# Kernel optimization log

Hardware: AMD Instinct MI355X
Metric: run time of the kernel (lower is better)

Reference implementation:

```python
import jax, jax.numpy as jnp
import numpy as np

D_MODEL = 2048
N_HEAD = 16
HEAD_DIM = D_MODEL // N_HEAD
FFN_DIM = 4 * D_MODEL
B, T = 2, 2048
EPS = float(np.finfo(np.float32).eps)  # torch nn.RMSNorm default eps


def _rmsnorm(x, w):
    return x * jax.lax.rsqrt(jnp.mean(x * x, axis=-1, keepdims=True) + EPS) * w


def _apply_rope(x, cos, sin):
    # x: (B,H,T,hd); cos/sin: (T,hd) with each frequency repeated twice
    cos_pair = cos[..., 0::2]
    sin_pair = sin[..., 0::2]
    x_even = x[..., 0::2]
    x_odd = x[..., 1::2]
    rot_even = x_even * cos_pair - x_odd * sin_pair
    rot_odd = x_odd * cos_pair + x_even * sin_pair
    # interleave back: (..., hd//2, 2) -> (..., hd)
    return jnp.stack([rot_even, rot_odd], axis=-1).reshape(x.shape)


def setup_inputs() -> dict:
    key = jax.random.key(0)
    ks = jax.random.split(key, 9)
    x = jax.random.normal(ks[0], (B, T, D_MODEL), dtype=jnp.float32)
    # real RoPE cache: freqs repeated twice along last axis (interleaved-pair)
    inv_freq = 1.0 / (10000.0 ** (np.arange(0, HEAD_DIM, 2, dtype=np.float32) / HEAD_DIM))
    ang = np.arange(T, dtype=np.float32)[:, None] * inv_freq[None, :]  # (T, hd/2)
    ang2 = np.repeat(ang, 2, axis=-1)  # (T, hd)
    rope_cache = jnp.stack([jnp.cos(jnp.asarray(ang2)), jnp.sin(jnp.asarray(ang2))], axis=0)
    s = 0.02
    return {
        "x": x,
        "rope_cache": rope_cache,
        "attn_norm_w": jnp.ones((D_MODEL,), jnp.float32),
        "qkv_w": s * jax.random.normal(ks[1], (3 * D_MODEL, D_MODEL), jnp.float32),
        "q_norm_w": jnp.ones((HEAD_DIM,), jnp.float32),
        "k_norm_w": jnp.ones((HEAD_DIM,), jnp.float32),
        "out_proj_w": s * jax.random.normal(ks[2], (D_MODEL, D_MODEL), jnp.float32),
        "mlp_norm_w": jnp.ones((D_MODEL,), jnp.float32),
        "mlp_in_w": s * jax.random.normal(ks[3], (FFN_DIM, D_MODEL), jnp.float32),
        "mlp_out_w": s * jax.random.normal(ks[4], (D_MODEL, FFN_DIM), jnp.float32),
    }


def reference(x, rope_cache, attn_norm_w, qkv_w, q_norm_w, k_norm_w,
              out_proj_w, mlp_norm_w, mlp_in_w, mlp_out_w):
    cos, sin = rope_cache[0], rope_cache[1]
    b, t, d = x.shape
    h = _rmsnorm(x, attn_norm_w)
    qkv = h @ qkv_w.T  # (B,T,3D)
    q, k, v = jnp.split(qkv, 3, axis=-1)
    q = q.reshape(b, t, N_HEAD, HEAD_DIM).transpose(0, 2, 1, 3)
    k = k.reshape(b, t, N_HEAD, HEAD_DIM).transpose(0, 2, 1, 3)
    v = v.reshape(b, t, N_HEAD, HEAD_DIM).transpose(0, 2, 1, 3)
    q = _rmsnorm(_apply_rope(q, cos, sin), q_norm_w)
    k = _rmsnorm(_apply_rope(k, cos, sin), k_norm_w)
    scale = 1.0 / jnp.sqrt(jnp.float32(HEAD_DIM))
    scores = jnp.einsum('bhqd,bhkd->bhqk', q, k) * scale
    causal = jnp.tril(jnp.ones((t, t), dtype=bool))
    scores = jnp.where(causal, scores, -jnp.inf)
    attn = jax.nn.softmax(scores, axis=-1)
    attn_out = jnp.einsum('bhqk,bhkd->bhqd', attn, v)
    attn_out = attn_out.transpose(0, 2, 1, 3).reshape(b, t, d)
    x = x + attn_out @ out_proj_w.T
    m = _rmsnorm(x, mlp_norm_w) @ mlp_in_w.T
    m = jnp.square(jax.nn.relu(m))
    return x + m @ mlp_out_w.T
```

## Files before the change

### kernel.cpp

```cpp
#include <hip/hip_runtime.h>
#include <stdint.h>

#define TT 2048
#define DM 2048
#define NH 16
#define HD 128
#define FFN 8192
#define MR 4096
#define EPSF 1.1920928955078125e-07f
#define NEGBIG (-1.0e30f)

typedef __attribute__((ext_vector_type(8))) short short8;
typedef __attribute__((ext_vector_type(4))) float f32x4;
typedef unsigned short u16;
typedef unsigned int u32;

__device__ __forceinline__ float bf2f(u32 u) {
    return __uint_as_float((u & 0xffffu) << 16);
}
__device__ __forceinline__ u16 f2bf(float f) {
    u32 x = __float_as_uint(f);
    return (u16)((x + 0x7fffu + ((x >> 16) & 1u)) >> 16);
}
__device__ __forceinline__ void load8f(const u16* p, float* v) {
    uint4 d = *(const uint4*)p;
    v[0] = bf2f(d.x); v[1] = bf2f(d.x >> 16);
    v[2] = bf2f(d.y); v[3] = bf2f(d.y >> 16);
    v[4] = bf2f(d.z); v[5] = bf2f(d.z >> 16);
    v[6] = bf2f(d.w); v[7] = bf2f(d.w >> 16);
}
__device__ __forceinline__ void load8f32(const float* p, float* v) {
    float4 a = *(const float4*)p, b = *(const float4*)(p + 4);
    v[0]=a.x; v[1]=a.y; v[2]=a.z; v[3]=a.w; v[4]=b.x; v[5]=b.y; v[6]=b.z; v[7]=b.w;
}
__device__ __forceinline__ void store8bf(u16* p, const float* v) {
    uint4 o;
    o.x = (u32)f2bf(v[0]) | ((u32)f2bf(v[1]) << 16);
    o.y = (u32)f2bf(v[2]) | ((u32)f2bf(v[3]) << 16);
    o.z = (u32)f2bf(v[4]) | ((u32)f2bf(v[5]) << 16);
    o.w = (u32)f2bf(v[6]) | ((u32)f2bf(v[7]) << 16);
    *(uint4*)p = o;
}
__device__ __forceinline__ uint4 cvt8_f32_bf16(const float* p) {
    float4 a = *(const float4*)p, b = *(const float4*)(p + 4);
    uint4 o;
    o.x = (u32)f2bf(a.x) | ((u32)f2bf(a.y) << 16);
    o.y = (u32)f2bf(a.z) | ((u32)f2bf(a.w) << 16);
    o.z = (u32)f2bf(b.x) | ((u32)f2bf(b.y) << 16);
    o.w = (u32)f2bf(b.z) | ((u32)f2bf(b.w) << 16);
    return o;
}
__device__ __forceinline__ void gload_lds16(const void* g, void* l) {
    __builtin_amdgcn_global_load_lds((const __attribute__((address_space(1))) u32*)g,
                                     (__attribute__((address_space(3))) u32*)l, 16, 0, 0);
}

__global__ __launch_bounds__(256)
void cvt_w(const float* __restrict__ S, u16* __restrict__ D) {
    size_t i = ((size_t)blockIdx.x * 256 + threadIdx.x) * 8;
    *(uint4*)(D + i) = cvt8_f32_bf16(S + i);
}

__global__ __launch_bounds__(256)
void rmsnorm_k(const float* __restrict__ X, const float* __restrict__ W, u16* __restrict__ O) {
    const int row = blockIdx.x, tid = threadIdx.x;
    float v[8];
    load8f32(X + (size_t)row * DM + tid * 8, v);
    float ssq = 0.f;
#pragma unroll
    for (int i = 0; i < 8; ++i) ssq += v[i] * v[i];
#pragma unroll
    for (int d = 1; d < 64; d <<= 1) ssq += __shfl_xor(ssq, d);
    __shared__ float red[4];
    if ((tid & 63) == 0) red[tid >> 6] = ssq;
    __syncthreads();
    ssq = red[0] + red[1] + red[2] + red[3];
    const float inv = rsqrtf(ssq * (1.f / DM) + EPSF);
    float wv[8], o[8];
    load8f32(W + tid * 8, wv);
#pragma unroll
    for (int i = 0; i < 8; ++i) o[i] = v[i] * inv * wv[i];
    store8bf(O + (size_t)row * DM + tid * 8, o);
}

template<int EPI>
__global__ __launch_bounds__(256)
void gemm_bt(const u16* __restrict__ A, const u16* __restrict__ Bw,
             const float* __restrict__ Res, void* __restrict__ Cp,
             int M, int N, int K, int ldb) {
    __shared__ alignas(16) u16 As[128 * 32];
    __shared__ alignas(16) u16 Bs[128 * 32];
    const int tid = threadIdx.x;
    const int lane = tid & 63, w = tid >> 6;
    const int quad = lane >> 4, col = lane & 15;
    const int n0 = blockIdx.x * 128, m0 = blockIdx.y * 128;
    const int wm = (w >> 1) * 64, wn = (w & 1) * 64;

    const int c0 = tid, c1 = tid + 256;
    const int ar0 = c0 >> 2, aq0 = (c0 & 3) ^ ((ar0 >> 1) & 3);
    const int ar1 = c1 >> 2, aq1 = (c1 & 3) ^ ((ar1 >> 1) & 3);
    const u16* agp0 = A  + (size_t)(m0 + ar0) * K + aq0 * 8;
    const u16* agp1 = A  + (size_t)(m0 + ar1) * K + aq1 * 8;
    const u16* bgp0 = Bw + (size_t)(n0 + ar0) * ldb + aq0 * 8;
    const u16* bgp1 = Bw + (size_t)(n0 + ar1) * ldb + aq1 * 8;
    u16* al0 = As + c0 * 8; u16* al1 = As + c1 * 8;
    u16* bl0 = Bs + c0 * 8; u16* bl1 = Bs + c1 * 8;

    int aoff[4], boff[4];
#pragma unroll
    for (int i = 0; i < 4; ++i) {
        int r = wm + i * 16 + col;
        aoff[i] = r * 32 + (quad ^ ((r >> 1) & 3)) * 8;
        r = wn + i * 16 + col;
        boff[i] = r * 32 + (quad ^ ((r >> 1) & 3)) * 8;
    }

    f32x4 acc[4][4];
#pragma unroll
    for (int i = 0; i < 4; ++i)
#pragma unroll
        for (int j = 0; j < 4; ++j) acc[i][j] = (f32x4){0.f, 0.f, 0.f, 0.f};

    for (int kt = 0; kt < K; kt += 32) {
        __syncthreads();
        gload_lds16(agp0 + kt, al0);
        gload_lds16(agp1 + kt, al1);
        gload_lds16(bgp0 + kt, bl0);
        gload_lds16(bgp1 + kt, bl1);
        __syncthreads();
        short8 af[4], bfr[4];
#pragma unroll
        for (int i = 0; i < 4; ++i) af[i] = *(const short8*)(As + aoff[i]);
#pragma unroll
        for (int i = 0; i < 4; ++i) bfr[i] = *(const short8*)(Bs + boff[i]);
#pragma unroll
        for (int mi = 0; mi < 4; ++mi)
#pragma unroll
            for (int ni = 0; ni < 4; ++ni)
                acc[mi][ni] = __builtin_amdgcn_mfma_f32_16x16x32_bf16(af[mi], bfr[ni], acc[mi][ni], 0, 0, 0);
    }

#pragma unroll
    for (int mi = 0; mi < 4; ++mi)
#pragma unroll
        for (int ni = 0; ni < 4; ++ni) {
            const int rbase = m0 + wm + mi * 16 + quad * 4;
            const int cc = n0 + wn + ni * 16 + col;
#pragma unroll
            for (int rr = 0; rr < 4; ++rr) {
                float v = acc[mi][ni][rr];
                size_t idx = (size_t)(rbase + rr) * N + cc;
                if (EPI == 0) ((u16*)Cp)[idx] = f2bf(v);
                else if (EPI == 1) { float t = fmaxf(v, 0.f); ((u16*)Cp)[idx] = f2bf(t * t); }
                else ((float*)Cp)[idx] = v + Res[idx];
            }
        }
}

template<int EPI>
__global__ __launch_bounds__(512, 2)
void gemm_big(const u16* __restrict__ A, const u16* __restrict__ Bw,
              void* __restrict__ Cp, int M, int N, int K, int ldb) {
    __shared__ alignas(16) u16 As[4][256 * 32];
    __shared__ alignas(16) u16 Bs[4][256 * 32];
    const int tid = threadIdx.x;
    const int lane = tid & 63, w = tid >> 6;
    const int wr = w >> 2, wc = w & 3;
    const int quad = lane >> 4, colL = lane & 15;

    const int nbx = N >> 8;
    const int nwg = gridDim.x;
    const int cpx = nwg >> 3;
    const int bid = blockIdx.x;
    const int swz = (bid & 7) * cpx + (bid >> 3);
    const int by = swz / nbx, bx = swz - by * nbx;
    const int m0 = by << 8, n0 = bx << 8;

    const int r0 = tid >> 2,       q0 = (tid & 3) ^ ((r0 >> 1) & 3);
    const int p1 = tid + 512;
    const int r1 = p1 >> 2,        q1 = (p1 & 3) ^ ((r1 >> 1) & 3);
    const u16* agp0 = A  + (size_t)(m0 + r0) * K   + q0 * 8;
    const u16* agp1 = A  + (size_t)(m0 + r1) * K   + q1 * 8;
    const u16* bgp0 = Bw + (size_t)(n0 + r0) * ldb + q0 * 8;
    const u16* bgp1 = Bw + (size_t)(n0 + r1) * ldb + q1 * 8;
    const int l0 = tid * 8, l1 = p1 * 8;

    int aoff[8], boff[4];
#pragma unroll
    for (int mi = 0; mi < 8; ++mi) {
        int r = wr * 128 + mi * 16 + colL;
        aoff[mi] = r * 32 + (quad ^ ((r >> 1) & 3)) * 8;
    }
#pragma unroll
    for (int ni = 0; ni < 4; ++ni) {
        int r = wc * 64 + ni * 16 + colL;
        boff[ni] = r * 32 + (quad ^ ((r >> 1) & 3)) * 8;
    }

    f32x4 acc[8][4];
#pragma unroll
    for (int i = 0; i < 8; ++i)
#pragma unroll
        for (int j = 0; j < 4; ++j) acc[i][j] = (f32x4){0.f, 0.f, 0.f, 0.f};

    const int KT = K >> 5;

#define GB_STAGE(s) { const int _b = (s) & 3; const size_t _ko = (size_t)(s) * 32; \
    gload_lds16(agp0 + _ko, &As[_b][l0]); \
    gload_lds16(agp1 + _ko, &As[_b][l1]); \
    gload_lds16(bgp0 + _ko, &Bs[_b][l0]); \
    gload_lds16(bgp1 + _ko, &Bs[_b][l1]); }

    GB_STAGE(0);
    GB_STAGE(1);
    GB_STAGE(2);

    for (int t = 0; t < KT; ++t) {
        const int rem = KT - 1 - t;
        if (rem >= 2)      asm volatile("s_waitcnt vmcnt(8)" ::: "memory");
        else if (rem == 1) asm volatile("s_waitcnt vmcnt(4)" ::: "memory");
        else               asm volatile("s_waitcnt vmcnt(0)" ::: "memory");
        __builtin_amdgcn_s_barrier();
        if (t + 3 < KT) GB_STAGE(t + 3);
        const u16* ab = As[t & 3];
        const u16* bb = Bs[t & 3];
        short8 af[8], bfr[4];
#pragma unroll
        for (int mi = 0; mi < 8; ++mi) af[mi] = *(const short8*)(ab + aoff[mi]);
#pragma unroll
        for (int ni = 0; ni < 4; ++ni) bfr[ni] = *(const short8*)(bb + boff[ni]);
        __builtin_amdgcn_s_setprio(1);
#pragma unroll
        for (int mi = 0; mi < 8; ++mi)
#pragma unroll
            for (int ni = 0; ni < 4; ++ni)
                acc[mi][ni] = __builtin_amdgcn_mfma_f32_16x16x32_bf16(af[mi], bfr[ni], acc[mi][ni], 0, 0, 0);
        __builtin_amdgcn_s_setprio(0);
        __builtin_amdgcn_sched_barrier(0);
    }
#undef GB_STAGE

#pragma unroll
    for (int mi = 0; mi < 8; ++mi)
#pragma unroll
        for (int ni = 0; ni < 4; ++ni) {
            const int rbase = m0 + wr * 128 + mi * 16 + quad * 4;
            const int cc = n0 + wc * 64 + ni * 16 + colL;
#pragma unroll
            for (int rr = 0; rr < 4; ++rr) {
                float v = acc[mi][ni][rr];
                size_t idx = (size_t)(rbase + rr) * N + cc;
                if (EPI == 0) ((u16*)Cp)[idx] = f2bf(v);
                else { float tq = fmaxf(v, 0.f); ((u16*)Cp)[idx] = f2bf(tq * tq); }
            }
        }
}

__global__ __launch_bounds__(256)
void rope_split_k(const u16* __restrict__ QKV, const float* __restrict__ RC,
                  const float* __restrict__ QW, const float* __restrict__ KW,
                  u16* __restrict__ Qo, u16* __restrict__ Ko, u16* __restrict__ Vo) {
    const int row = blockIdx.x;
    const int t = row & (TT - 1), b = row >> 11;
    const int tid = threadIdx.x, h = tid >> 4, j = tid & 15;
    const size_t qb = (size_t)row * (3 * DM) + h * HD + j * 8;
    float q[8], k[8], cs[8], sn[8];
    load8f(QKV + qb, q);
    load8f(QKV + qb + DM, k);
    uint4 vv = *(const uint4*)(QKV + qb + 2 * DM);
    load8f32(RC + (size_t)t * HD + j * 8, cs);
    load8f32(RC + (size_t)(TT + t) * HD + j * 8, sn);
    float qr[8], kr[8];
#pragma unroll
    for (int p = 0; p < 4; ++p) {
        float c = cs[2 * p], s = sn[2 * p];
        qr[2*p]   = q[2*p]   * c - q[2*p+1] * s;
        qr[2*p+1] = q[2*p+1] * c + q[2*p]   * s;
        kr[2*p]   = k[2*p]   * c - k[2*p+1] * s;
        kr[2*p+1] = k[2*p+1] * c + k[2*p]   * s;
    }
    float sq = 0.f, sk = 0.f;
#pragma unroll
    for (int i = 0; i < 8; ++i) { sq += qr[i] * qr[i]; sk += kr[i] * kr[i]; }
#pragma unroll
    for (int d = 1; d < 16; d <<= 1) { sq += __shfl_xor(sq, d); sk += __shfl_xor(sk, d); }
    const float iq = rsqrtf(sq * (1.f / HD) + EPSF);
    const float ik = rsqrtf(sk * (1.f / HD) + EPSF);
    float qw[8], kw[8], oq[8], ok[8];
    load8f32(QW + j * 8, qw); load8f32(KW + j * 8, kw);
#pragma unroll
    for (int i = 0; i < 8; ++i) { oq[i] = qr[i] * iq * qw[i]; ok[i] = kr[i] * ik * kw[i]; }
    const size_t ob = ((size_t)(b * NH + h) * TT + t) * HD + j * 8;
    store8bf(Qo + ob, oq);
    store8bf(Ko + ob, ok);
    *(uint4*)(Vo + ob) = vv;
}

__global__ __launch_bounds__(256)
void transpose_v(const u16* __restrict__ V, u16* __restrict__ Vt) {
    __shared__ alignas(16) u16 tile[64][72];
    const int bh = blockIdx.z;
    const int t0 = blockIdx.x * 64, d0 = blockIdx.y * 64;
    const int tid = threadIdx.x;
#pragma unroll
    for (int i = 0; i < 2; ++i) {
        int c = i * 256 + tid;
        int r = c >> 3, cc = (c & 7) * 8;
        *(uint4*)(&tile[r][cc]) = *(const uint4*)(V + ((size_t)bh * TT + t0 + r) * HD + d0 + cc);
    }
    __syncthreads();
#pragma unroll
    for (int i = 0; i < 2; ++i) {
        int c = i * 256 + tid;
        int dc = c >> 3, rr = (c & 7) * 8;
        u16 tmp[8];
#pragma unroll
        for (int kk = 0; kk < 8; ++kk) tmp[kk] = tile[rr + kk][dc];
        uint4 o;
        o.x = (u32)tmp[0] | ((u32)tmp[1] << 16);
        o.y = (u32)tmp[2] | ((u32)tmp[3] << 16);
        o.z = (u32)tmp[4] | ((u32)tmp[5] << 16);
        o.w = (u32)tmp[6] | ((u32)tmp[7] << 16);
        *(uint4*)(Vt + ((size_t)bh * HD + d0 + dc) * TT + t0 + rr) = o;
    }
}

__global__ __launch_bounds__(256)
void attn_k(const u16* __restrict__ Q, const u16* __restrict__ Kg,
            const u16* __restrict__ Vt, u16* __restrict__ O) {
    __shared__ alignas(16) u16 k_lds[2][64 * 128];
    __shared__ alignas(16) u16 v_lds[2][128 * 64];
    __shared__ alignas(16) u16 p_lds[4 * 16 * 72];
    const int qt = gridDim.x - 1 - blockIdx.x;
    const int bh = blockIdx.y;
    const int tid = threadIdx.x, lane = tid & 63, w = tid >> 6;
    const int quad = lane >> 4, col = lane & 15;
    const int qbase = qt * 64;
    const int qrow = qbase + w * 16 + col;

    short8 qf[4];
    const u16* qp = Q + ((size_t)bh * TT + qrow) * HD;
#pragma unroll
    for (int s = 0; s < 4; ++s) qf[s] = *(const short8*)(qp + s * 32 + quad * 8);

    const u16* kp[4]; const u16* vp[4];
#pragma unroll
    for (int i = 0; i < 4; ++i) {
        int lin = i * 256 + tid;
        int r = lin >> 4, sl = lin & 15;
        int gq = sl ^ (r & 15);
        kp[i] = Kg + ((size_t)bh * TT + r) * HD + gq * 8;
    }
#pragma unroll
    for (int i = 0; i < 4; ++i) {
        int lin = i * 256 + tid;
        int r = lin >> 3, sl = lin & 7;
        int gq = sl ^ (r & 7);
        vp[i] = Vt + ((size_t)bh * HD + r) * TT + gq * 8;
    }

    f32x4 oacc[8];
#pragma unroll
    for (int i = 0; i < 8; ++i) oacc[i] = (f32x4){0.f, 0.f, 0.f, 0.f};
    float mrow[4] = {NEGBIG, NEGBIG, NEGBIG, NEGBIG};
    float lrow[4] = {0.f, 0.f, 0.f, 0.f};
    const float scale = 0.08838834764831845f;

    u16* kcur = k_lds[0]; u16* knxt = k_lds[1];
    u16* vcur = v_lds[0]; u16* vnxt = v_lds[1];
#pragma unroll
    for (int i = 0; i < 4; ++i) gload_lds16(kp[i], kcur + (i * 256 + tid) * 8);
#pragma unroll
    for (int i = 0; i < 4; ++i) gload_lds16(vp[i], vcur + (i * 256 + tid) * 8);

    for (int kt = 0; kt <= qt; ++kt) {
        const int kb = kt * 64;
        __syncthreads();

        if (kt < qt) {
            const int kb2 = kb + 64;
#pragma unroll
            for (int i = 0; i < 4; ++i) gload_lds16(kp[i] + (size_t)kb2 * HD, knxt + (i * 256 + tid) * 8);
#pragma unroll
            for (int i = 0; i < 4; ++i) gload_lds16(vp[i] + kb2, vnxt + (i * 256 + tid) * 8);
        }

        f32x4 sfr[4];
#pragma unroll
        for (int ni = 0; ni < 4; ++ni) sfr[ni] = (f32x4){0.f, 0.f, 0.f, 0.f};
        __builtin_amdgcn_s_setprio(1);
#pragma unroll
        for (int ni = 0; ni < 4; ++ni) {
            const int r = ni * 16 + col;
#pragma unroll
            for (int s = 0; s < 4; ++s) {
                int sl = (s * 4 + quad) ^ (r & 15);
                short8 kf = *(const short8*)(kcur + r * 128 + sl * 8);
                sfr[ni] = __builtin_amdgcn_mfma_f32_16x16x32_bf16(qf[s], kf, sfr[ni], 0, 0, 0);
            }
        }
        __builtin_amdgcn_s_setprio(0);
        const bool diag = (kt == qt);
#pragma unroll
        for (int ni = 0; ni < 4; ++ni) {
            const int key = kb + ni * 16 + col;
#pragma unroll
            for (int rr = 0; rr < 4; ++rr) {
                float v = sfr[ni][rr] * scale;
                int qv = qbase + w * 16 + quad * 4 + rr;
                if (diag && key > qv) v = NEGBIG;
                sfr[ni][rr] = v;
            }
        }
        float mx[4];
#pragma unroll
        for (int rr = 0; rr < 4; ++rr)
            mx[rr] = fmaxf(fmaxf(sfr[0][rr], sfr[1][rr]), fmaxf(sfr[2][rr], sfr[3][rr]));
#pragma unroll
        for (int d = 1; d < 16; d <<= 1)
#pragma unroll
            for (int rr = 0; rr < 4; ++rr) mx[rr] = fmaxf(mx[rr], __shfl_xor(mx[rr], d));
        if (__any((mx[0] > mrow[0]) || (mx[1] > mrow[1]) ||
                  (mx[2] > mrow[2]) || (mx[3] > mrow[3]))) {
#pragma unroll
            for (int rr = 0; rr < 4; ++rr) {
                float mn = fmaxf(mrow[rr], mx[rr]);
                float a = __expf(mrow[rr] - mn);
                mrow[rr] = mn;
                lrow[rr] *= a;
#pragma unroll
                for (int i = 0; i < 8; ++i) oacc[i][rr] *= a;
            }
        }
        float rs[4] = {0.f, 0.f, 0.f, 0.f};
#pragma unroll
        for (int ni = 0; ni < 4; ++ni)
#pragma unroll
            for (int rr = 0; rr < 4; ++rr) {
                float p = __expf(sfr[ni][rr] - mrow[rr]);
                sfr[ni][rr] = p;
                rs[rr] += p;
            }
#pragma unroll
        for (int d = 1; d < 16; d <<= 1)
#pragma unroll
            for (int rr = 0; rr < 4; ++rr) rs[rr] += __shfl_xor(rs[rr], d);
#pragma unroll
        for (int rr = 0; rr < 4; ++rr) lrow[rr] += rs[rr];
#pragma unroll
        for (int ni = 0; ni < 4; ++ni)
#pragma unroll
            for (int rr = 0; rr < 4; ++rr)
                p_lds[(w * 16 + quad * 4 + rr) * 72 + ni * 16 + col] = f2bf(sfr[ni][rr]);
        __builtin_amdgcn_s_setprio(1);
#pragma unroll
        for (int ks = 0; ks < 2; ++ks) {
            short8 pa = *(const short8*)(p_lds + (w * 16 + col) * 72 + ks * 32 + quad * 8);
#pragma unroll
            for (int di = 0; di < 8; ++di) {
                int r = di * 16 + col;
                int sl = (ks * 4 + quad) ^ (r & 7);
                short8 vb = *(const short8*)(vcur + r * 64 + sl * 8);
                oacc[di] = __builtin_amdgcn_mfma_f32_16x16x32_bf16(pa, vb, oacc[di], 0, 0, 0);
            }
        }
        __builtin_amdgcn_s_setprio(0);
        { u16* t = kcur; kcur = knxt; knxt = t; }
        { u16* t = vcur; vcur = vnxt; vnxt = t; }
    }
    const int b = bh >> 4, h = bh & 15;
#pragma unroll
    for (int di = 0; di < 8; ++di)
#pragma unroll
        for (int rr = 0; rr < 4; ++rr) {
            int trow = qbase + w * 16 + quad * 4 + rr;
            float ov = oacc[di][rr] / lrow[rr];
            O[((size_t)(b * TT + trow)) * DM + h * HD + di * 16 + col] = f2bf(ov);
        }
}

extern "C" void kernel_launch(void* const* d_in, const int* in_sizes, int n_in,
                              void* d_out, int out_size, void* d_ws, size_t ws_size,
                              hipStream_t stream) {
    const float* x    = (const float*)d_in[0];
    const float* rc   = (const float*)d_in[1];
    const float* anw  = (const float*)d_in[2];
    const float* qkvw = (const float*)d_in[3];
    const float* qnw  = (const float*)d_in[4];
    const float* knw  = (const float*)d_in[5];
    const float* opw  = (const float*)d_in[6];
    const float* mnw  = (const float*)d_in[7];
    const float* miw  = (const float*)d_in[8];
    const float* mow  = (const float*)d_in[9];

    char* ws = (char*)d_ws;
    u16* hbuf = (u16*)(ws);
    u16* Wq   = (u16*)(ws + (16ll  << 20));
    u16* Wmi  = (u16*)(ws + (16ll  << 20));
    u16* vt   = (u16*)(ws + (16ll  << 20));
    u16* aout = (u16*)(ws + (32ll  << 20));
    u16* Wmo  = (u16*)(ws + (48ll  << 20));
    u16* qkv  = (u16*)(ws + (48ll  << 20));
    u16* mbuf = (u16*)(ws + (80ll  << 20));
    u16* qh   = (u16*)(ws + (96ll  << 20));
    u16* Wo   = (u16*)(ws + (112ll << 20));
    u16* kh   = (u16*)(ws + (112ll << 20));
    u16* vh   = (u16*)(ws);
    float* xo = (float*)d_out;

    rmsnorm_k<<<MR, 256, 0, stream>>>(x, anw, hbuf);
    cvt_w<<<6144, 256, 0, stream>>>(qkvw, Wq);
    gemm_big<0><<<384, 512, 0, stream>>>(hbuf, Wq, qkv, MR, 3 * DM, DM, DM);
    rope_split_k<<<MR, 256, 0, stream>>>(qkv, rc, qnw, knw, qh, kh, vh);
    transpose_v<<<dim3(32, 2, 32), 256, 0, stream>>>(vh, vt);
    attn_k<<<dim3(32, 32), 256, 0, stream>>>(qh, kh, vt, aout);
    cvt_w<<<2048, 256, 0, stream>>>(opw, Wo);
    cvt_w<<<8192, 256, 0, stream>>>(mow, Wmo);
    gemm_bt<2><<<dim3(16, 32), 256, 0, stream>>>(aout, Wo, x, xo, MR, DM, DM, DM);
    rmsnorm_k<<<MR, 256, 0, stream>>>(xo, mnw, hbuf);
    cvt_w<<<8192, 256, 0, stream>>>(miw, Wmi);
    gemm_big<1><<<256, 512, 0, stream>>>(hbuf, Wmi, mbuf, MR, FFN / 2, DM, DM);
    gemm_bt<2><<<dim3(16, 32), 256, 0, stream>>>(mbuf, Wmo, xo, xo, MR, DM, FFN / 2, FFN);
    gemm_big<1><<<256, 512, 0, stream>>>(hbuf, Wmi + (size_t)(FFN / 2) * DM, mbuf, MR, FFN / 2, DM, DM);
    gemm_bt<2><<<dim3(16, 32), 256, 0, stream>>>(mbuf, Wmo + FFN / 2, xo, xo, MR, DM, FFN / 2, FFN);
}
```

Baseline: 1.047 ms.

## Pipeline residual GEMMs with 4-stage LDS ring and enlarge attention query tile

```diff
diff --git a/kernel.cpp b/kernel.cpp
--- a/kernel.cpp
+++ b/kernel.cpp
@@ -84,12 +84,12 @@
 }
 
 template<int EPI>
-__global__ __launch_bounds__(256)
-void gemm_bt(const u16* __restrict__ A, const u16* __restrict__ Bw,
-             const float* __restrict__ Res, void* __restrict__ Cp,
-             int M, int N, int K, int ldb) {
-    __shared__ alignas(16) u16 As[128 * 32];
-    __shared__ alignas(16) u16 Bs[128 * 32];
+__global__ __launch_bounds__(256, 2)
+void gemm_ring(const u16* __restrict__ A, const u16* __restrict__ Bw,
+               const float* __restrict__ Res, void* __restrict__ Cp,
+               int M, int N, int K, int ldb) {
+    __shared__ alignas(16) u16 As[4][128 * 32];
+    __shared__ alignas(16) u16 Bs[4][128 * 32];
     const int tid = threadIdx.x;
     const int lane = tid & 63, w = tid >> 6;
     const int quad = lane >> 4, col = lane & 15;
@@ -103,8 +103,7 @@
     const u16* agp1 = A  + (size_t)(m0 + ar1) * K + aq1 * 8;
     const u16* bgp0 = Bw + (size_t)(n0 + ar0) * ldb + aq0 * 8;
     const u16* bgp1 = Bw + (size_t)(n0 + ar1) * ldb + aq1 * 8;
-    u16* al0 = As + c0 * 8; u16* al1 = As + c1 * 8;
-    u16* bl0 = Bs + c0 * 8; u16* bl1 = Bs + c1 * 8;
+    const int l0 = c0 * 8, l1 = c1 * 8;
 
     int aoff[4], boff[4];
 #pragma unroll
@@ -121,24 +120,42 @@
 #pragma unroll
         for (int j = 0; j < 4; ++j) acc[i][j] = (f32x4){0.f, 0.f, 0.f, 0.f};
 
-    for (int kt = 0; kt < K; kt += 32) {
-        __syncthreads();
-        gload_lds16(agp0 + kt, al0);
-        gload_lds16(agp1 + kt, al1);
-        gload_lds16(bgp0 + kt, bl0);
-        gload_lds16(bgp1 + kt, bl1);
-        __syncthreads();
+    const int KT = K >> 5;
+
+#define GR_STAGE(s) { const int _b = (s) & 3; const size_t _ko = (size_t)(s) * 32; \
+    gload_lds16(agp0 + _ko, &As[_b][l0]); \
+    gload_lds16(agp1 + _ko, &As[_b][l1]); \
+    gload_lds16(bgp0 + _ko, &Bs[_b][l0]); \
+    gload_lds16(bgp1 + _ko, &Bs[_b][l1]); }
+
+    GR_STAGE(0);
+    GR_STAGE(1);
+    GR_STAGE(2);
+
+    for (int t = 0; t < KT; ++t) {
+        const int rem = KT - 1 - t;
+        if (rem >= 2)      asm volatile("s_waitcnt vmcnt(8)" ::: "memory");
+        else if (rem == 1) asm volatile("s_waitcnt vmcnt(4)" ::: "memory");
+        else               asm volatile("s_waitcnt vmcnt(0)" ::: "memory");
+        __builtin_amdgcn_s_barrier();
+        if (t + 3 < KT) GR_STAGE(t + 3);
+        const u16* ab = As[t & 3];
+        const u16* bb = Bs[t & 3];
         short8 af[4], bfr[4];
 #pragma unroll
-        for (int i = 0; i < 4; ++i) af[i] = *(const short8*)(As + aoff[i]);
-#pragma unroll
-        for (int i = 0; i < 4; ++i) bfr[i] = *(const short8*)(Bs + boff[i]);
+        for (int i = 0; i < 4; ++i) af[i] = *(const short8*)(ab + aoff[i]);
+#pragma unroll
+        for (int i = 0; i < 4; ++i) bfr[i] = *(const short8*)(bb + boff[i]);
+        __builtin_amdgcn_s_setprio(1);
 #pragma unroll
         for (int mi = 0; mi < 4; ++mi)
 #pragma unroll
             for (int ni = 0; ni < 4; ++ni)
                 acc[mi][ni] = __builtin_amdgcn_mfma_f32_16x16x32_bf16(af[mi], bfr[ni], acc[mi][ni], 0, 0, 0);
-    }
+        __builtin_amdgcn_s_setprio(0);
+        __builtin_amdgcn_sched_barrier(0);
+    }
+#undef GR_STAGE
 
 #pragma unroll
     for (int mi = 0; mi < 4; ++mi)
@@ -151,7 +168,7 @@
                 float v = acc[mi][ni][rr];
                 size_t idx = (size_t)(rbase + rr) * N + cc;
                 if (EPI == 0) ((u16*)Cp)[idx] = f2bf(v);
-                else if (EPI == 1) { float t = fmaxf(v, 0.f); ((u16*)Cp)[idx] = f2bf(t * t); }
+                else if (EPI == 1) { float t2 = fmaxf(v, 0.f); ((u16*)Cp)[idx] = f2bf(t2 * t2); }
                 else ((float*)Cp)[idx] = v + Res[idx];
             }
         }
@@ -325,23 +342,26 @@
     }
 }
 
-__global__ __launch_bounds__(256)
+__global__ __launch_bounds__(256, 2)
 void attn_k(const u16* __restrict__ Q, const u16* __restrict__ Kg,
             const u16* __restrict__ Vt, u16* __restrict__ O) {
     __shared__ alignas(16) u16 k_lds[2][64 * 128];
     __shared__ alignas(16) u16 v_lds[2][128 * 64];
-    __shared__ alignas(16) u16 p_lds[4 * 16 * 72];
+    __shared__ alignas(16) u16 p_lds[128 * 40];
     const int qt = gridDim.x - 1 - blockIdx.x;
     const int bh = blockIdx.y;
     const int tid = threadIdx.x, lane = tid & 63, w = tid >> 6;
     const int quad = lane >> 4, col = lane & 15;
-    const int qbase = qt * 64;
-    const int qrow = qbase + w * 16 + col;
-
-    short8 qf[4];
-    const u16* qp = Q + ((size_t)bh * TT + qrow) * HD;
-#pragma unroll
-    for (int s = 0; s < 4; ++s) qf[s] = *(const short8*)(qp + s * 32 + quad * 8);
+    const int qbase = qt * 128;
+    const int wq = qbase + w * 32;
+
+    short8 qf[2][4];
+#pragma unroll
+    for (int sub = 0; sub < 2; ++sub) {
+        const u16* qp = Q + ((size_t)bh * TT + wq + sub * 16 + col) * HD;
+#pragma unroll
+        for (int s = 0; s < 4; ++s) qf[sub][s] = *(const short8*)(qp + s * 32 + quad * 8);
+    }
 
     const u16* kp[4]; const u16* vp[4];
 #pragma unroll
@@ -359,11 +379,16 @@
         vp[i] = Vt + ((size_t)bh * HD + r) * TT + gq * 8;
     }
 
-    f32x4 oacc[8];
-#pragma unroll
-    for (int i = 0; i < 8; ++i) oacc[i] = (f32x4){0.f, 0.f, 0.f, 0.f};
-    float mrow[4] = {NEGBIG, NEGBIG, NEGBIG, NEGBIG};
-    float lrow[4] = {0.f, 0.f, 0.f, 0.f};
+    f32x4 oacc[2][8];
+#pragma unroll
+    for (int s = 0; s < 2; ++s)
+#pragma unroll
+        for (int i = 0; i < 8; ++i) oacc[s][i] = (f32x4){0.f, 0.f, 0.f, 0.f};
+    float mrow[2][4], lrow[2][4];
+#pragma unroll
+    for (int s = 0; s < 2; ++s)
+#pragma unroll
+        for (int r = 0; r < 4; ++r) { mrow[s][r] = NEGBIG; lrow[s][r] = 0.f; }
     const float scale = 0.08838834764831845f;
 
     u16* kcur = k_lds[0]; u16* knxt = k_lds[1];
@@ -373,11 +398,12 @@
 #pragma unroll
     for (int i = 0; i < 4; ++i) gload_lds16(vp[i], vcur + (i * 256 + tid) * 8);
 
-    for (int kt = 0; kt <= qt; ++kt) {
+    const int ktmax = 2 * qt + 1;
+    for (int kt = 0; kt <= ktmax; ++kt) {
         const int kb = kt * 64;
         __syncthreads();
 
-        if (kt < qt) {
+        if (kt < ktmax) {
             const int kb2 = kb + 64;
 #pragma unroll
             for (int i = 0; i < 4; ++i) gload_lds16(kp[i] + (size_t)kb2 * HD, knxt + (i * 256 + tid) * 8);
@@ -385,9 +411,11 @@
             for (int i = 0; i < 4; ++i) gload_lds16(vp[i] + kb2, vnxt + (i * 256 + tid) * 8);
         }
 
-        f32x4 sfr[4];
-#pragma unroll
-        for (int ni = 0; ni < 4; ++ni) sfr[ni] = (f32x4){0.f, 0.f, 0.f, 0.f};
+        f32x4 sfr[2][4];
+#pragma unroll
+        for (int s = 0; s < 2; ++s)
+#pragma unroll
+            for (int ni = 0; ni < 4; ++ni) sfr[s][ni] = (f32x4){0.f, 0.f, 0.f, 0.f};
         __builtin_amdgcn_s_setprio(1);
 #pragma unroll
         for (int ni = 0; ni < 4; ++ni) {
@@ -396,87 +424,118 @@
             for (int s = 0; s < 4; ++s) {
                 int sl = (s * 4 + quad) ^ (r & 15);
                 short8 kf = *(const short8*)(kcur + r * 128 + sl * 8);
-                sfr[ni] = __builtin_amdgcn_mfma_f32_16x16x32_bf16(qf[s], kf, sfr[ni], 0, 0, 0);
+                sfr[0][ni] = __builtin_amdgcn_mfma_f32_16x16x32_bf16(qf[0][s], kf, sfr[0][ni], 0, 0, 0);
+                sfr[1][ni] = __builtin_amdgcn_mfma_f32_16x16x32_bf16(qf[1][s], kf, sfr[1][ni], 0, 0, 0);
             }
         }
         __builtin_amdgcn_s_setprio(0);
-        const bool diag = (kt == qt);
-#pragma unroll
-        for (int ni = 0; ni < 4; ++ni) {
-            const int key = kb + ni * 16 + col;
-#pragma unroll
-            for (int rr = 0; rr < 4; ++rr) {
-                float v = sfr[ni][rr] * scale;
-                int qv = qbase + w * 16 + quad * 4 + rr;
-                if (diag && key > qv) v = NEGBIG;
-                sfr[ni][rr] = v;
+#pragma unroll
+        for (int sub = 0; sub < 2; ++sub)
+#pragma unroll
+            for (int ni = 0; ni < 4; ++ni) {
+                const int key = kb + ni * 16 + col;
+#pragma unroll
+                for (int rr = 0; rr < 4; ++rr) {
+                    float v = sfr[sub][ni][rr] * scale;
+                    int qv = wq + sub * 16 + quad * 4 + rr;
+                    if (key > qv) v = NEGBIG;
+                    sfr[sub][ni][rr] = v;
+                }
             }
+        float mx[2][4];
+#pragma unroll
+        for (int sub = 0; sub < 2; ++sub)
+#pragma unroll
+            for (int rr = 0; rr < 4; ++rr)
+                mx[sub][rr] = fmaxf(fmaxf(sfr[sub][0][rr], sfr[sub][1][rr]),
+                                    fmaxf(sfr[sub][2][rr], sfr[sub][3][rr]));
+#pragma unroll
+        for (int d = 1; d < 16; d <<= 1)
+#pragma unroll
+            for (int sub = 0; sub < 2; ++sub)
+#pragma unroll
+                for (int rr = 0; rr < 4; ++rr) mx[sub][rr] = fmaxf(mx[sub][rr], __shfl_xor(mx[sub][rr], d));
+        bool grew = false;
+#pragma unroll
+        for (int sub = 0; sub < 2; ++sub)
+#pragma unroll
+            for (int rr = 0; rr < 4; ++rr) grew = grew || (mx[sub][rr] > mrow[sub][rr]);
+        if (__any(grew)) {
+#pragma unroll
+            for (int sub = 0; sub < 2; ++sub)
+#pragma unroll
+                for (int rr = 0; rr < 4; ++rr) {
+                    float mn = fmaxf(mrow[sub][rr], mx[sub][rr]);
+                    float a = __expf(mrow[sub][rr] - mn);
+                    mrow[sub][rr] = mn;
+                    lrow[sub][rr] *= a;
+#pragma unroll
+                    for (int i = 0; i < 8; ++i) oacc[sub][i][rr] *= a;
+                }
         }
-        float mx[4];
-#pragma unroll
-        for (int rr = 0; rr < 4; ++rr)
-            mx[rr] = fmaxf(fmaxf(sfr[0][rr], sfr[1][rr]), fmaxf(sfr[2][rr], sfr[3][rr]));
+        float rs[2][4];
+#pragma unroll
+        for (int s = 0; s < 2; ++s)
+#pragma unroll
+            for (int r = 0; r < 4; ++r) rs[s][r] = 0.f;
+#pragma unroll
+        for (int sub = 0; sub < 2; ++sub)
+#pragma unroll
+            for (int ni = 0; ni < 4; ++ni)
+#pragma unroll
+                for (int rr = 0; rr < 4; ++rr) {
+                    float p = __expf(sfr[sub][ni][rr] - mrow[sub][rr]);
+                    sfr[sub][ni][rr] = p;
+                    rs[sub][rr] += p;
+                }
 #pragma unroll
         for (int d = 1; d < 16; d <<= 1)
 #pragma unroll
-            for (int rr = 0; rr < 4; ++rr) mx[rr] = fmaxf(mx[rr], __shfl_xor(mx[rr], d));
-        if (__any((mx[0] > mrow[0]) || (mx[1] > mrow[1]) ||
-                  (mx[2] > mrow[2]) || (mx[3] > mrow[3]))) {
-#pragma unroll
-            for (int rr = 0; rr < 4; ++rr) {
-                float mn = fmaxf(mrow[rr], mx[rr]);
-                float a = __expf(mrow[rr] - mn);
-                mrow[rr] = mn;
-                lrow[rr] *= a;
-#pragma unroll
-                for (int i = 0; i < 8; ++i) oacc[i][rr] *= a;
-            }
-        }
-        float rs[4] = {0.f, 0.f, 0.f, 0.f};
-#pragma unroll
-        for (int ni = 0; ni < 4; ++ni)
-#pragma unroll
-            for (int rr = 0; rr < 4; ++rr) {
-                float p = __expf(sfr[ni][rr] - mrow[rr]);
-                sfr[ni][rr] = p;
-                rs[rr] += p;
-            }
-#pragma unroll
-        for (int d = 1; d < 16; d <<= 1)
-#pragma unroll
-            for (int rr = 0; rr < 4; ++rr) rs[rr] += __shfl_xor(rs[rr], d);
-#pragma unroll
-        for (int rr = 0; rr < 4; ++rr) lrow[rr] += rs[rr];
-#pragma unroll
-        for (int ni = 0; ni < 4; ++ni)
-#pragma unroll
-            for (int rr = 0; rr < 4; ++rr)
-                p_lds[(w * 16 + quad * 4 + rr) * 72 + ni * 16 + col] = f2bf(sfr[ni][rr]);
-        __builtin_amdgcn_s_setprio(1);
+            for (int sub = 0; sub < 2; ++sub)
+#pragma unroll
+                for (int rr = 0; rr < 4; ++rr) rs[sub][rr] += __shfl_xor(rs[sub][rr], d);
+#pragma unroll
+        for (int sub = 0; sub < 2; ++sub)
+#pragma unroll
+            for (int rr = 0; rr < 4; ++rr) lrow[sub][rr] += rs[sub][rr];
 #pragma unroll
         for (int ks = 0; ks < 2; ++ks) {
-            short8 pa = *(const short8*)(p_lds + (w * 16 + col) * 72 + ks * 32 + quad * 8);
+#pragma unroll
+            for (int sub = 0; sub < 2; ++sub)
+#pragma unroll
+                for (int nio = 0; nio < 2; ++nio) {
+                    const int ni = ks * 2 + nio;
+#pragma unroll
+                    for (int rr = 0; rr < 4; ++rr)
+                        p_lds[(w * 32 + sub * 16 + quad * 4 + rr) * 40 + nio * 16 + col] = f2bf(sfr[sub][ni][rr]);
+                }
+            short8 pa0 = *(const short8*)(p_lds + (w * 32 + col) * 40 + quad * 8);
+            short8 pa1 = *(const short8*)(p_lds + (w * 32 + 16 + col) * 40 + quad * 8);
+            __builtin_amdgcn_s_setprio(1);
 #pragma unroll
             for (int di = 0; di < 8; ++di) {
                 int r = di * 16 + col;
                 int sl = (ks * 4 + quad) ^ (r & 7);
                 short8 vb = *(const short8*)(vcur + r * 64 + sl * 8);
-                oacc[di] = __builtin_amdgcn_mfma_f32_16x16x32_bf16(pa, vb, oacc[di], 0, 0, 0);
+                oacc[0][di] = __builtin_amdgcn_mfma_f32_16x16x32_bf16(pa0, vb, oacc[0][di], 0, 0, 0);
+                oacc[1][di] = __builtin_amdgcn_mfma_f32_16x16x32_bf16(pa1, vb, oacc[1][di], 0, 0, 0);
             }
+            __builtin_amdgcn_s_setprio(0);
         }
-        __builtin_amdgcn_s_setprio(0);
         { u16* t = kcur; kcur = knxt; knxt = t; }
         { u16* t = vcur; vcur = vnxt; vnxt = t; }
     }
-    const int b = bh >> 4, h = bh & 15;
-#pragma unroll
-    for (int di = 0; di < 8; ++di)
-#pragma unroll
-        for (int rr = 0; rr < 4; ++rr) {
-            int trow = qbase + w * 16 + quad * 4 + rr;
-            float ov = oacc[di][rr] / lrow[rr];
-            O[((size_t)(b * TT + trow)) * DM + h * HD + di * 16 + col] = f2bf(ov);
-        }
+    const int b = bh >> 4, hh = bh & 15;
+#pragma unroll
+    for (int sub = 0; sub < 2; ++sub)
+#pragma unroll
+        for (int di = 0; di < 8; ++di)
+#pragma unroll
+            for (int rr = 0; rr < 4; ++rr) {
+                int trow = wq + sub * 16 + quad * 4 + rr;
+                float ov = oacc[sub][di][rr] / lrow[sub][rr];
+                O[((size_t)(b * TT + trow)) * DM + hh * HD + di * 16 + col] = f2bf(ov);
+            }
 }
 
 extern "C" void kernel_launch(void* const* d_in, const int* in_sizes, int n_in,
@@ -513,14 +572,14 @@
     gemm_big<0><<<384, 512, 0, stream>>>(hbuf, Wq, qkv, MR, 3 * DM, DM, DM);
     rope_split_k<<<MR, 256, 0, stream>>>(qkv, rc, qnw, knw, qh, kh, vh);
     transpose_v<<<dim3(32, 2, 32), 256, 0, stream>>>(vh, vt);
-    attn_k<<<dim3(32, 32), 256, 0, stream>>>(qh, kh, vt, aout);
+    attn_k<<<dim3(16, 32), 256, 0, stream>>>(qh, kh, vt, aout);
     cvt_w<<<2048, 256, 0, stream>>>(opw, Wo);
     cvt_w<<<8192, 256, 0, stream>>>(mow, Wmo);
-    gemm_bt<2><<<dim3(16, 32), 256, 0, stream>>>(aout, Wo, x, xo, MR, DM, DM, DM);
+    gemm_ring<2><<<dim3(16, 32), 256, 0, stream>>>(aout, Wo, x, xo, MR, DM, DM, DM);
     rmsnorm_k<<<MR, 256, 0, stream>>>(xo, mnw, hbuf);
     cvt_w<<<8192, 256, 0, stream>>>(miw, Wmi);
     gemm_big<1><<<256, 512, 0, stream>>>(hbuf, Wmi, mbuf, MR, FFN / 2, DM, DM);
-    gemm_bt<2><<<dim3(16, 32), 256, 0, stream>>>(mbuf, Wmo, xo, xo, MR, DM, FFN / 2, FFN);
+    gemm_ring<2><<<dim3(16, 32), 256, 0, stream>>>(mbuf, Wmo, xo, xo, MR, DM, FFN / 2, FFN);
     gemm_big<1><<<256, 512, 0, stream>>>(hbuf, Wmi + (size_t)(FFN / 2) * DM, mbuf, MR, FFN / 2, DM, DM);
-    gemm_bt<2><<<dim3(16, 32), 256, 0, stream>>>(mbuf, Wmo + FFN / 2, xo, xo, MR, DM, FFN / 2, FFN);
-}
+    gemm_ring<2><<<dim3(16, 32), 256, 0, stream>>>(mbuf, Wmo + FFN / 2, xo, xo, MR, DM, FFN / 2, FFN);
+}
```

After: 995.7 us. 4.9% less time.
